# Performance work log

Measured on AMD Instinct MI355X. Metric: run time of the kernel, lower is better.

The kernel has to match this reference:

```python
import jax, jax.numpy as jnp
import numpy as np

B, T, D, H = 2, 2048, 1024, 16
DH = D // H

def setup_inputs() -> dict:
    key = jax.random.key(0)
    ks = jax.random.split(key, 5)
    s = 1.0 / np.sqrt(D)
    return {
        "x": jax.random.normal(ks[0], (B, T, D), dtype=jnp.float32),
        "w_q": jax.random.normal(ks[1], (D, D), dtype=jnp.float32) * s,
        "w_k": jax.random.normal(ks[2], (D, D), dtype=jnp.float32) * s,
        "w_v": jax.random.normal(ks[3], (D, D), dtype=jnp.float32) * s,
        "w_o": jax.random.normal(ks[4], (D, D), dtype=jnp.float32) * s,
    }

def reference(x, w_q, w_k, w_v, w_o):
    # Linear(bias=False): y = x @ W.T
    q = jnp.einsum('btd,ed->bte', x, w_q).reshape(B, T, H, DH).transpose(0, 2, 1, 3)
    k = jnp.einsum('btd,ed->bte', x, w_k).reshape(B, T, H, DH).transpose(0, 2, 1, 3)
    v = jnp.einsum('btd,ed->bte', x, w_v).reshape(B, T, H, DH).transpose(0, 2, 1, 3)
    scores = jnp.einsum('bhqd,bhkd->bhqk', q, k) / np.sqrt(DH)  # [B,H,T,T]
    causal = jnp.triu(jnp.ones((T, T), dtype=bool), k=1)
    scores = jnp.where(causal[None, None, :, :], -jnp.inf, scores)
    attn = jax.nn.softmax(scores, axis=-1)
    ctx = jnp.einsum('bhqk,bhkd->bhqd', attn, v)
    ctx = ctx.transpose(0, 2, 1, 3).reshape(B, T, D)
    out = jnp.einsum('btd,ed->bte', ctx, w_o)
    return out
```

## Files before the change

### kernel.cpp

```cpp
#include <hip/hip_runtime.h>
#include <hip/hip_bf16.h>

typedef __bf16 bf16_t;
typedef __attribute__((ext_vector_type(8))) __bf16 bf16x8;
typedef __attribute__((ext_vector_type(4))) __bf16 bf16x4;
typedef __attribute__((ext_vector_type(4))) float f32x4;
typedef __attribute__((ext_vector_type(16))) float f32x16;
typedef __attribute__((ext_vector_type(2))) int i32x2;

#define B_ 2
#define T_ 2048
#define D_ 1024
#define H_ 16
#define DH_ 64
#define RS_ 3072

static __device__ __forceinline__ f32x4 mfma16(bf16x8 a, bf16x8 b, f32x4 c) {
  return __builtin_amdgcn_mfma_f32_16x16x32_bf16(a, b, c, 0, 0, 0);
}
static __device__ __forceinline__ f32x16 mfma32(bf16x8 a, bf16x8 b, f32x16 c) {
  return __builtin_amdgcn_mfma_f32_32x32x16_bf16(a, b, c, 0, 0, 0);
}
static __device__ __forceinline__ void gld16(const bf16_t* g, bf16_t* l) {
  __builtin_amdgcn_global_load_lds(
      (const __attribute__((address_space(1))) unsigned int*)g,
      (__attribute__((address_space(3))) unsigned int*)l, 16, 0, 0);
}
static __device__ __forceinline__ unsigned lds_addr(const bf16_t* p) {
  return (unsigned)(uintptr_t)(const __attribute__((address_space(3))) bf16_t*)p;
}
static __device__ __forceinline__ i32x2 tr64(unsigned a) {
  i32x2 d;
  asm volatile("ds_read_b64_tr_b16 %0, %1" : "=v"(d) : "v"(a));
  return d;
}
static __device__ __forceinline__ i32x2 tr64o(unsigned a) {
  i32x2 d;
  asm volatile("ds_read_b64_tr_b16 %0, %1 offset:128" : "=v"(d) : "v"(a));
  return d;
}
static __device__ __forceinline__ unsigned pk2(float lo, float hi2) {
  unsigned short a = __builtin_bit_cast(unsigned short, (bf16_t)lo);
  unsigned short b = __builtin_bit_cast(unsigned short, (bf16_t)hi2);
  return (unsigned)a | ((unsigned)b << 16);
}

#define WAITV4 { asm volatile("s_waitcnt vmcnt(4)" ::: "memory"); __builtin_amdgcn_sched_barrier(0); }
#define WAITV8 { asm volatile("s_waitcnt vmcnt(8)" ::: "memory"); __builtin_amdgcn_sched_barrier(0); }
#define WAITV0 { asm volatile("s_waitcnt vmcnt(0)" ::: "memory"); __builtin_amdgcn_sched_barrier(0); }
#define BAR    { __builtin_amdgcn_s_barrier(); __builtin_amdgcn_sched_barrier(0); }
#define WAITL0 { asm volatile("s_waitcnt lgkmcnt(0)" ::: "memory"); __builtin_amdgcn_sched_barrier(0); }

__global__ __launch_bounds__(256) void cvt_x(const float* __restrict__ in,
                                             bf16_t* __restrict__ out, int n4) {
  int i = blockIdx.x * 256 + threadIdx.x;
  if (i >= n4) return;
  float4 f = reinterpret_cast<const float4*>(in)[i];
  bf16x4 o;
  o[0] = (bf16_t)f.x; o[1] = (bf16_t)f.y; o[2] = (bf16_t)f.z; o[3] = (bf16_t)f.w;
  reinterpret_cast<bf16x4*>(out)[i] = o;
}

__global__ __launch_bounds__(256) void cvt_w4(const float* __restrict__ w0,
                                              const float* __restrict__ w1,
                                              const float* __restrict__ w2,
                                              const float* __restrict__ w3,
                                              bf16_t* __restrict__ out, int n4each) {
  const float* in = blockIdx.y == 0 ? w0 : blockIdx.y == 1 ? w1 : blockIdx.y == 2 ? w2 : w3;
  bf16_t* o = out + (size_t)blockIdx.y * (size_t)n4each * 4;
  int i = blockIdx.x * 256 + threadIdx.x;
  if (i >= n4each) return;
  float4 f = reinterpret_cast<const float4*>(in)[i];
  bf16x4 v;
  v[0] = (bf16_t)f.x; v[1] = (bf16_t)f.y; v[2] = (bf16_t)f.z; v[3] = (bf16_t)f.w;
  reinterpret_cast<bf16x4*>(o)[i] = v;
}

template <bool STORE_F32, bool QSCALE>
__global__ __launch_bounds__(256) void gemm_nt(const bf16_t* __restrict__ A,
                                               const bf16_t* __restrict__ Bm,
                                               void* __restrict__ Cv,
                                               int M, int N, int K) {
  __shared__ __align__(16) bf16_t As[3][128 * 32];
  __shared__ __align__(16) bf16_t Bs[3][128 * 32];
  const int tid = threadIdx.x, lane = tid & 63, wave = tid >> 6;
  const int l15 = lane & 15;
  const int brow = blockIdx.y * 128, bcol = blockIdx.x * 128;
  const int row0 = (wave >> 1) * 64, col0 = (wave & 1) * 64;
  const float cscale = (QSCALE && bcol < 1024) ? 0.18033688011112042f : 1.0f;

  f32x4 acc[4][4];
#pragma unroll
  for (int m = 0; m < 4; ++m)
#pragma unroll
    for (int n = 0; n < 4; ++n) acc[m][n] = f32x4{0.f, 0.f, 0.f, 0.f};

  const int nst = K >> 5;
  const int srow = tid >> 2;
  const int sc8 = (tid & 3) * 8;
  auto stage = [&](int bi, int ks) {
    const int k0 = ks * 32;
#pragma unroll
    for (int i = 0; i < 2; ++i)
      gld16(A + (size_t)(brow + 64 * i + srow) * K + k0 + sc8,
            &As[bi][2048 * i + 512 * wave]);
#pragma unroll
    for (int i = 0; i < 2; ++i)
      gld16(Bm + (size_t)(bcol + 64 * i + srow) * K + k0 + sc8,
            &Bs[bi][2048 * i + 512 * wave]);
  };

  stage(0, 0);
  stage(1, 1);

#pragma unroll 1
  for (int ks = 0; ks < nst; ++ks) {
    if (ks + 1 < nst) { WAITV4 } else { WAITV0 }
    BAR;
    if (ks + 2 < nst) stage((ks + 2) % 3, ks + 2);

    const bf16_t* Ab = &As[ks % 3][0];
    const bf16_t* Bb = &Bs[ks % 3][0];
    const int ko = (lane >> 4) * 8;
    bf16x8 af[4], bfr[4];
#pragma unroll
    for (int m = 0; m < 4; ++m)
      af[m] = *(const bf16x8*)&Ab[(row0 + 16 * m + l15) * 32 + ko];
#pragma unroll
    for (int n = 0; n < 4; ++n)
      bfr[n] = *(const bf16x8*)&Bb[(col0 + 16 * n + l15) * 32 + ko];
    WAITL0;
#pragma unroll
    for (int m = 0; m < 4; ++m)
#pragma unroll
      for (int n = 0; n < 4; ++n) acc[m][n] = mfma16(af[m], bfr[n], acc[m][n]);
  }

  const int crow = brow + row0 + (lane >> 4) * 4;
  const int ccol = bcol + col0 + l15;
#pragma unroll
  for (int m = 0; m < 4; ++m)
#pragma unroll
    for (int n = 0; n < 4; ++n)
#pragma unroll
      for (int r = 0; r < 4; ++r) {
        size_t idx = (size_t)(crow + 16 * m + r) * N + (ccol + 16 * n);
        float v = acc[m][n][r] * cscale;
        if (STORE_F32) reinterpret_cast<float*>(Cv)[idx] = v;
        else reinterpret_cast<bf16_t*>(Cv)[idx] = (bf16_t)v;
      }
}

#define CROW(r) ((((r) & 3) + 8 * ((r) >> 2)) + 4 * hi)

__global__ __launch_bounds__(128, 2) void attn_fwd(const bf16_t* __restrict__ qkv,
                                                   bf16_t* __restrict__ ctx) {
  __shared__ __align__(128) bf16_t KV[3][2][64 * 64];
  const int tid = threadIdx.x;
  const int lane = tid & 63;
  const int wv = tid >> 6;
  const int bh = blockIdx.x, p = blockIdx.y;
  const int b = bh >> 4, h = bh & 15;
  const bf16_t* Qg = qkv + (size_t)b * T_ * RS_ + h * DH_;
  const bf16_t* Kg = Qg + 1024;
  const bf16_t* Vg = Qg + 2048;
  bf16_t* Cg = ctx + (size_t)b * T_ * D_ + h * DH_;

  const int hi = lane >> 5;
  const int l31 = lane & 31;
  const int l15 = lane & 15;

  auto stage = [&](int bi, int kt) {
    bf16_t* Kb = &KV[bi][0][0];
    bf16_t* Vb = &KV[bi][1][0];
#pragma unroll
    for (int i = 0; i < 4; ++i) {
      int c2 = i * 128 + tid;
      int r = c2 >> 3, g8 = (c2 & 7) ^ (r & 7);
      gld16(Kg + (size_t)(kt * 64 + r) * RS_ + g8 * 8, Kb + i * 1024 + wv * 512);
    }
#pragma unroll
    for (int i = 0; i < 4; ++i) {
      int c2 = i * 128 + tid;
      int pn = c2 >> 7, k = (c2 >> 1) & 63, half = c2 & 1;
      gld16(Vg + (size_t)(kt * 64 + k) * RS_ + pn * 16 + half * 8, Vb + i * 1024 + wv * 512);
    }
  };

#pragma unroll 1
  for (int phase = 0; phase < 2; ++phase) {
    const int c = phase ? (63 - 2 * p - wv) : (2 * p + wv);
    const int q0 = c * 32;
    const int nkt = phase ? (32 - p) : (p + 1);

    BAR;
    stage(0, 0);
    stage(1, 1);

    bf16x8 qf[4];
#pragma unroll
    for (int d = 0; d < 4; ++d)
      qf[d] = *(const bf16x8*)&Qg[(size_t)(q0 + l31) * RS_ + d * 16 + hi * 8];

    f32x16 o[2];
#pragma unroll
    for (int n = 0; n < 2; ++n)
#pragma unroll
      for (int r = 0; r < 16; ++r) o[n][r] = 0.f;
    float mrow = -1e30f, lsum = 0.f;

#pragma unroll 1
    for (int kt = 0; kt < nkt; ++kt) {
      if (kt + 1 < nkt) { WAITV8 } else { WAITV0 }
      BAR;
      if (kt + 2 < nkt) stage((kt + 2) % 3, kt + 2);

      const bf16_t* Kb = &KV[kt % 3][0][0];
      bf16x8 kf[2][4];
#pragma unroll
      for (int t = 0; t < 2; ++t)
#pragma unroll
        for (int d = 0; d < 4; ++d) {
          int row = 32 * t + l31;
          int col = ((d * 2 + hi) ^ (row & 7)) * 8;
          kf[t][d] = *(const bf16x8*)&Kb[row * 64 + col];
        }
      bf16x8 vf[2][4];
      {
        unsigned vb = lds_addr(&KV[kt % 3][1][0]);
#pragma unroll
        for (int n2 = 0; n2 < 2; ++n2)
#pragma unroll
          for (int ks = 0; ks < 4; ++ks) {
            int pn = 2 * n2 + (l31 >> 4);
            int k0 = ks * 16 + hi * 8;
            unsigned a = vb + pn * 2048 + k0 * 32 + l15 * 8;
            i32x2 lo = tr64(a);
            i32x2 hi4 = tr64o(a);
            union { unsigned u[4]; bf16x8 v; } uu;
            uu.u[0] = (unsigned)lo[0]; uu.u[1] = (unsigned)lo[1];
            uu.u[2] = (unsigned)hi4[0]; uu.u[3] = (unsigned)hi4[1];
            vf[n2][ks] = uu.v;
          }
      }
      WAITL0;

      f32x16 st[2];
#pragma unroll
      for (int t = 0; t < 2; ++t) {
#pragma unroll
        for (int r = 0; r < 16; ++r) st[t][r] = 0.f;
#pragma unroll
        for (int d = 0; d < 4; ++d) st[t] = mfma32(kf[t][d], qf[d], st[t]);
      }
      if (kt == nkt - 1) {
#pragma unroll
        for (int t = 0; t < 2; ++t)
#pragma unroll
          for (int r = 0; r < 16; ++r)
            if (kt * 64 + 32 * t + CROW(r) > q0 + l31) st[t][r] = -1e30f;
      }
      float pm = -1e30f;
#pragma unroll
      for (int t = 0; t < 2; ++t)
#pragma unroll
        for (int r = 0; r < 16; ++r) pm = fmaxf(pm, st[t][r]);
      pm = fmaxf(pm, __shfl_xor(pm, 32));
      if (!__all(pm - mrow <= 11.0f)) {
        float mn = fmaxf(mrow, pm);
        float scl = exp2f(mrow - mn);
        mrow = mn;
        lsum *= scl;
#pragma unroll
        for (int r = 0; r < 16; ++r) {
          float sr = __shfl(scl, CROW(r));
          o[0][r] *= sr;
          o[1][r] *= sr;
        }
      }
      float ps = 0.f;
#pragma unroll
      for (int t = 0; t < 2; ++t)
#pragma unroll
        for (int r = 0; r < 16; ++r) {
          float e = exp2f(st[t][r] - mrow);
          st[t][r] = e;
          ps += e;
        }
      ps += __shfl_xor(ps, 32);
      lsum += ps;
      unsigned pk[2][8];
#pragma unroll
      for (int t = 0; t < 2; ++t)
#pragma unroll
        for (int j = 0; j < 8; ++j) pk[t][j] = pk2(st[t][2 * j], st[t][2 * j + 1]);
#pragma unroll
      for (int ks = 0; ks < 4; ++ks) {
        const int t = ks >> 1, rb = (ks & 1) * 4;
        unsigned s0 = hi ? pk[t][rb] : pk[t][rb + 2];
        unsigned s1 = hi ? pk[t][rb + 1] : pk[t][rb + 3];
        unsigned r0 = (unsigned)__shfl_xor((int)s0, 32);
        unsigned r1 = (unsigned)__shfl_xor((int)s1, 32);
        union { unsigned u[4]; bf16x8 v; } w;
        if (hi == 0) {
          w.u[0] = pk[t][rb]; w.u[1] = pk[t][rb + 1]; w.u[2] = r0; w.u[3] = r1;
        } else {
          w.u[0] = r0; w.u[1] = r1; w.u[2] = pk[t][rb + 2]; w.u[3] = pk[t][rb + 3];
        }
        o[0] = mfma32(w.v, vf[0][ks], o[0]);
        o[1] = mfma32(w.v, vf[1][ks], o[1]);
      }
    }

#pragma unroll
    for (int r = 0; r < 16; ++r) {
      float li = __shfl(lsum, CROW(r));
      float inv = 1.0f / li;
      int qrow = q0 + CROW(r);
#pragma unroll
      for (int n2 = 0; n2 < 2; ++n2)
        Cg[(size_t)qrow * D_ + n2 * 32 + l31] = (bf16_t)(o[n2][r] * inv);
    }
  }
}

extern "C" void kernel_launch(void* const* d_in, const int* in_sizes, int n_in,
                              void* d_out, int out_size, void* d_ws, size_t ws_size,
                              hipStream_t stream) {
  const float* x   = (const float*)d_in[0];
  const float* w_q = (const float*)d_in[1];
  const float* w_k = (const float*)d_in[2];
  const float* w_v = (const float*)d_in[3];
  const float* w_o = (const float*)d_in[4];

  const int M = B_ * T_;
  const size_t XN = (size_t)M * D_;
  const size_t WN = (size_t)D_ * D_;

  bf16_t* ws = (bf16_t*)d_ws;
  bf16_t* xb   = ws;
  bf16_t* wqb  = xb + XN;
  bf16_t* wob  = wqb + 3 * WN;
  bf16_t* qkv  = wob + WN;
  bf16_t* ctx  = qkv + (size_t)M * RS_;

  cvt_x<<<(int)(XN / 4 / 256), 256, 0, stream>>>(x, xb, (int)(XN / 4));
  cvt_w4<<<dim3((int)(WN / 4 / 256), 4), 256, 0, stream>>>(w_q, w_k, w_v, w_o, wqb, (int)(WN / 4));

  gemm_nt<false, true><<<dim3(RS_ / 128, M / 128), 256, 0, stream>>>(xb, wqb, qkv, M, RS_, D_);

  attn_fwd<<<dim3(B_ * H_, 16), 128, 0, stream>>>(qkv, ctx);

  gemm_nt<true, false><<<dim3(D_ / 128, M / 128), 256, 0, stream>>>(ctx, wob, d_out, M, D_, D_);
}
```

Baseline: 155.6 us.

## Make attention waves independent with private double-buffered 32-key KV tiles

Reworks the causal attention kernel so each of 4 waves per block owns one 32-row query chunk. Each wave streams its own 32-key K/V tiles into a private double-buffered LDS region, with no block-wide barriers. This replaces the earlier scheme, where 2 waves shared 64-key tiles through a triple-buffered ring with barriers and ran two load-balancing phases. Chunks are assigned to blocks in even/odd interleaved order to spread causal work. The aim is to remove barrier stalls and raise waves per block. In exchange, K/V is no longer shared across waves, which multiplies global/L2 load traffic, and the smaller key tiles add per-iteration softmax overhead.

```diff
diff --git a/kernel.cpp b/kernel.cpp
--- a/kernel.cpp
+++ b/kernel.cpp
@@ -153,14 +153,16 @@
 
 #define CROW(r) ((((r) & 3) + 8 * ((r) >> 2)) + 4 * hi)
 
-__global__ __launch_bounds__(128, 2) void attn_fwd(const bf16_t* __restrict__ qkv,
+__global__ __launch_bounds__(256, 2) void attn_fwd(const bf16_t* __restrict__ qkv,
                                                    bf16_t* __restrict__ ctx) {
-  __shared__ __align__(128) bf16_t KV[3][2][64 * 64];
-  const int tid = threadIdx.x;
-  const int lane = tid & 63;
-  const int wv = tid >> 6;
-  const int bh = blockIdx.x, p = blockIdx.y;
+  __shared__ __align__(128) bf16_t KV[4][2][2][2048];
+  const int lane = threadIdx.x & 63;
+  const int wv = threadIdx.x >> 6;
+  const int bh = blockIdx.x, y = blockIdx.y;
   const int b = bh >> 4, h = bh & 15;
+  const int c = (y < 8) ? (8 * y + 2 * wv) : (63 - 8 * (y - 8) - 2 * wv);
+  const int q0 = c * 32;
+  const int nkt = c + 1;
   const bf16_t* Qg = qkv + (size_t)b * T_ * RS_ + h * DH_;
   const bf16_t* Kg = Qg + 1024;
   const bf16_t* Vg = Qg + 2048;
@@ -170,157 +172,138 @@
   const int l31 = lane & 31;
   const int l15 = lane & 15;
 
+  bf16_t* Kb[2] = {&KV[wv][0][0][0], &KV[wv][1][0][0]};
+  bf16_t* Vb[2] = {&KV[wv][0][1][0], &KV[wv][1][1][0]};
+
   auto stage = [&](int bi, int kt) {
-    bf16_t* Kb = &KV[bi][0][0];
-    bf16_t* Vb = &KV[bi][1][0];
 #pragma unroll
     for (int i = 0; i < 4; ++i) {
-      int c2 = i * 128 + tid;
+      int c2 = i * 64 + lane;
       int r = c2 >> 3, g8 = (c2 & 7) ^ (r & 7);
-      gld16(Kg + (size_t)(kt * 64 + r) * RS_ + g8 * 8, Kb + i * 1024 + wv * 512);
+      gld16(Kg + (size_t)(kt * 32 + r) * RS_ + g8 * 8, Kb[bi] + i * 512);
     }
 #pragma unroll
     for (int i = 0; i < 4; ++i) {
-      int c2 = i * 128 + tid;
-      int pn = c2 >> 7, k = (c2 >> 1) & 63, half = c2 & 1;
-      gld16(Vg + (size_t)(kt * 64 + k) * RS_ + pn * 16 + half * 8, Vb + i * 1024 + wv * 512);
+      int pn = i, k = lane >> 1, half = lane & 1;
+      gld16(Vg + (size_t)(kt * 32 + k) * RS_ + pn * 16 + half * 8, Vb[bi] + i * 512);
     }
   };
 
+  bf16x8 qf[4];
+#pragma unroll
+  for (int d = 0; d < 4; ++d)
+    qf[d] = *(const bf16x8*)&Qg[(size_t)(q0 + l31) * RS_ + d * 16 + hi * 8];
+
+  f32x16 o[2];
+#pragma unroll
+  for (int n = 0; n < 2; ++n)
+#pragma unroll
+    for (int r = 0; r < 16; ++r) o[n][r] = 0.f;
+  float mrow = -1e30f, lsum = 0.f;
+
+  stage(0, 0);
+  int cur = 0;
+
 #pragma unroll 1
-  for (int phase = 0; phase < 2; ++phase) {
-    const int c = phase ? (63 - 2 * p - wv) : (2 * p + wv);
-    const int q0 = c * 32;
-    const int nkt = phase ? (32 - p) : (p + 1);
-
-    BAR;
-    stage(0, 0);
-    stage(1, 1);
-
-    bf16x8 qf[4];
-#pragma unroll
-    for (int d = 0; d < 4; ++d)
-      qf[d] = *(const bf16x8*)&Qg[(size_t)(q0 + l31) * RS_ + d * 16 + hi * 8];
-
-    f32x16 o[2];
-#pragma unroll
-    for (int n = 0; n < 2; ++n)
-#pragma unroll
-      for (int r = 0; r < 16; ++r) o[n][r] = 0.f;
-    float mrow = -1e30f, lsum = 0.f;
-
-#pragma unroll 1
-    for (int kt = 0; kt < nkt; ++kt) {
-      if (kt + 1 < nkt) { WAITV8 } else { WAITV0 }
-      BAR;
-      if (kt + 2 < nkt) stage((kt + 2) % 3, kt + 2);
-
-      const bf16_t* Kb = &KV[kt % 3][0][0];
-      bf16x8 kf[2][4];
-#pragma unroll
-      for (int t = 0; t < 2; ++t)
-#pragma unroll
-        for (int d = 0; d < 4; ++d) {
-          int row = 32 * t + l31;
-          int col = ((d * 2 + hi) ^ (row & 7)) * 8;
-          kf[t][d] = *(const bf16x8*)&Kb[row * 64 + col];
+  for (int kt = 0; kt < nkt; ++kt) {
+    if (kt + 1 < nkt) {
+      stage(cur ^ 1, kt + 1);
+      WAITV8;
+    } else {
+      WAITV0;
+    }
+
+    bf16x8 kf[4];
+#pragma unroll
+    for (int d = 0; d < 4; ++d) {
+      int col = ((d * 2 + hi) ^ (l31 & 7)) * 8;
+      kf[d] = *(const bf16x8*)&Kb[cur][l31 * 64 + col];
+    }
+    bf16x8 vf[2][2];
+    {
+      unsigned vb = lds_addr(Vb[cur]);
+#pragma unroll
+      for (int n2 = 0; n2 < 2; ++n2)
+#pragma unroll
+        for (int ks = 0; ks < 2; ++ks) {
+          int pn = 2 * n2 + (l31 >> 4);
+          int k0 = ks * 16 + hi * 8;
+          unsigned a = vb + pn * 1024 + k0 * 32 + l15 * 8;
+          i32x2 lo = tr64(a);
+          i32x2 hi4 = tr64o(a);
+          union { unsigned u[4]; bf16x8 v; } uu;
+          uu.u[0] = (unsigned)lo[0]; uu.u[1] = (unsigned)lo[1];
+          uu.u[2] = (unsigned)hi4[0]; uu.u[3] = (unsigned)hi4[1];
+          vf[n2][ks] = uu.v;
         }
-      bf16x8 vf[2][4];
-      {
-        unsigned vb = lds_addr(&KV[kt % 3][1][0]);
-#pragma unroll
-        for (int n2 = 0; n2 < 2; ++n2)
-#pragma unroll
-          for (int ks = 0; ks < 4; ++ks) {
-            int pn = 2 * n2 + (l31 >> 4);
-            int k0 = ks * 16 + hi * 8;
-            unsigned a = vb + pn * 2048 + k0 * 32 + l15 * 8;
-            i32x2 lo = tr64(a);
-            i32x2 hi4 = tr64o(a);
-            union { unsigned u[4]; bf16x8 v; } uu;
-            uu.u[0] = (unsigned)lo[0]; uu.u[1] = (unsigned)lo[1];
-            uu.u[2] = (unsigned)hi4[0]; uu.u[3] = (unsigned)hi4[1];
-            vf[n2][ks] = uu.v;
-          }
+    }
+    WAITL0;
+
+    f32x16 st;
+#pragma unroll
+    for (int r = 0; r < 16; ++r) st[r] = 0.f;
+#pragma unroll
+    for (int d = 0; d < 4; ++d) st = mfma32(kf[d], qf[d], st);
+    if (kt == nkt - 1) {
+#pragma unroll
+      for (int r = 0; r < 16; ++r)
+        if (CROW(r) > l31) st[r] = -1e30f;
+    }
+    float pm = -1e30f;
+#pragma unroll
+    for (int r = 0; r < 16; ++r) pm = fmaxf(pm, st[r]);
+    pm = fmaxf(pm, __shfl_xor(pm, 32));
+    if (!__all(pm - mrow <= 11.0f)) {
+      float mn = fmaxf(mrow, pm);
+      float scl = exp2f(mrow - mn);
+      mrow = mn;
+      lsum *= scl;
+#pragma unroll
+      for (int r = 0; r < 16; ++r) {
+        float sr = __shfl(scl, CROW(r));
+        o[0][r] *= sr;
+        o[1][r] *= sr;
       }
-      WAITL0;
-
-      f32x16 st[2];
-#pragma unroll
-      for (int t = 0; t < 2; ++t) {
-#pragma unroll
-        for (int r = 0; r < 16; ++r) st[t][r] = 0.f;
-#pragma unroll
-        for (int d = 0; d < 4; ++d) st[t] = mfma32(kf[t][d], qf[d], st[t]);
+    }
+    float ps = 0.f;
+#pragma unroll
+    for (int r = 0; r < 16; ++r) {
+      float e = exp2f(st[r] - mrow);
+      st[r] = e;
+      ps += e;
+    }
+    ps += __shfl_xor(ps, 32);
+    lsum += ps;
+    unsigned pk[8];
+#pragma unroll
+    for (int j = 0; j < 8; ++j) pk[j] = pk2(st[2 * j], st[2 * j + 1]);
+#pragma unroll
+    for (int ks = 0; ks < 2; ++ks) {
+      const int rb = ks * 4;
+      unsigned s0 = hi ? pk[rb] : pk[rb + 2];
+      unsigned s1 = hi ? pk[rb + 1] : pk[rb + 3];
+      unsigned r0 = (unsigned)__shfl_xor((int)s0, 32);
+      unsigned r1 = (unsigned)__shfl_xor((int)s1, 32);
+      union { unsigned u[4]; bf16x8 v; } w;
+      if (hi == 0) {
+        w.u[0] = pk[rb]; w.u[1] = pk[rb + 1]; w.u[2] = r0; w.u[3] = r1;
+      } else {
+        w.u[0] = r0; w.u[1] = r1; w.u[2] = pk[rb + 2]; w.u[3] = pk[rb + 3];
       }
-      if (kt == nkt - 1) {
-#pragma unroll
-        for (int t = 0; t < 2; ++t)
-#pragma unroll
-          for (int r = 0; r < 16; ++r)
-            if (kt * 64 + 32 * t + CROW(r) > q0 + l31) st[t][r] = -1e30f;
-      }
-      float pm = -1e30f;
-#pragma unroll
-      for (int t = 0; t < 2; ++t)
-#pragma unroll
-        for (int r = 0; r < 16; ++r) pm = fmaxf(pm, st[t][r]);
-      pm = fmaxf(pm, __shfl_xor(pm, 32));
-      if (!__all(pm - mrow <= 11.0f)) {
-        float mn = fmaxf(mrow, pm);
-        float scl = exp2f(mrow - mn);
-        mrow = mn;
-        lsum *= scl;
-#pragma unroll
-        for (int r = 0; r < 16; ++r) {
-          float sr = __shfl(scl, CROW(r));
-          o[0][r] *= sr;
-          o[1][r] *= sr;
-        }
-      }
-      float ps = 0.f;
-#pragma unroll
-      for (int t = 0; t < 2; ++t)
-#pragma unroll
-        for (int r = 0; r < 16; ++r) {
-          float e = exp2f(st[t][r] - mrow);
-          st[t][r] = e;
-          ps += e;
-        }
-      ps += __shfl_xor(ps, 32);
-      lsum += ps;
-      unsigned pk[2][8];
-#pragma unroll
-      for (int t = 0; t < 2; ++t)
-#pragma unroll
-        for (int j = 0; j < 8; ++j) pk[t][j] = pk2(st[t][2 * j], st[t][2 * j + 1]);
-#pragma unroll
-      for (int ks = 0; ks < 4; ++ks) {
-        const int t = ks >> 1, rb = (ks & 1) * 4;
-        unsigned s0 = hi ? pk[t][rb] : pk[t][rb + 2];
-        unsigned s1 = hi ? pk[t][rb + 1] : pk[t][rb + 3];
-        unsigned r0 = (unsigned)__shfl_xor((int)s0, 32);
-        unsigned r1 = (unsigned)__shfl_xor((int)s1, 32);
-        union { unsigned u[4]; bf16x8 v; } w;
-        if (hi == 0) {
-          w.u[0] = pk[t][rb]; w.u[1] = pk[t][rb + 1]; w.u[2] = r0; w.u[3] = r1;
-        } else {
-          w.u[0] = r0; w.u[1] = r1; w.u[2] = pk[t][rb + 2]; w.u[3] = pk[t][rb + 3];
-        }
-        o[0] = mfma32(w.v, vf[0][ks], o[0]);
-        o[1] = mfma32(w.v, vf[1][ks], o[1]);
-      }
-    }
-
-#pragma unroll
-    for (int r = 0; r < 16; ++r) {
-      float li = __shfl(lsum, CROW(r));
-      float inv = 1.0f / li;
-      int qrow = q0 + CROW(r);
-#pragma unroll
-      for (int n2 = 0; n2 < 2; ++n2)
-        Cg[(size_t)qrow * D_ + n2 * 32 + l31] = (bf16_t)(o[n2][r] * inv);
-    }
+      o[0] = mfma32(w.v, vf[0][ks], o[0]);
+      o[1] = mfma32(w.v, vf[1][ks], o[1]);
+    }
+    cur ^= 1;
+  }
+
+#pragma unroll
+  for (int r = 0; r < 16; ++r) {
+    float li = __shfl(lsum, CROW(r));
+    float inv = 1.0f / li;
+    int qrow = q0 + CROW(r);
+#pragma unroll
+    for (int n2 = 0; n2 < 2; ++n2)
+      Cg[(size_t)qrow * D_ + n2 * 32 + l31] = (bf16_t)(o[n2][r] * inv);
   }
 }
 
@@ -349,7 +332,7 @@
 
   gemm_nt<false, true><<<dim3(RS_ / 128, M / 128), 256, 0, stream>>>(xb, wqb, qkv, M, RS_, D_);
 
-  attn_fwd<<<dim3(B_ * H_, 16), 128, 0, stream>>>(qkv, ctx);
+  attn_fwd<<<dim3(B_ * H_, 16), 256, 0, stream>>>(qkv, ctx);
 
   gemm_nt<true, false><<<dim3(D_ / 128, M / 128), 256, 0, stream>>>(ctx, wob, d_out, M, D_, D_);
 }
```

Result: no change. 153.5 us (-1.3%).
